# Optimization experiments

Measured on AMD Instinct MI355X. Metric: run time of the kernel, lower is better.

## Reference

```python
import jax, jax.numpy as jnp
import numpy as np

N_NODES = 50000
N_EDGES = 1600000
IN_DIM, HID, HEADS, OUT_DIM = 128, 32, 4, 16
NEG_SLOPE = 0.2  # DGL GATConv default


def setup_inputs() -> dict:
    key = jax.random.key(0)
    ks = jax.random.split(key, 12)
    features = jax.random.normal(ks[0], (N_NODES, IN_DIM), dtype=jnp.float32)
    src = jax.random.randint(ks[1], (N_EDGES,), 0, N_NODES, dtype=jnp.int32)
    dst = jax.random.randint(ks[2], (N_EDGES,), 0, N_NODES, dtype=jnp.int32)
    # layer 1 params (xavier-style scale)
    W1 = jax.random.normal(ks[3], (IN_DIM, HEADS * HID), dtype=jnp.float32) * (2.0 / (IN_DIM + HEADS * HID)) ** 0.5
    al1 = jax.random.normal(ks[4], (HEADS, HID), dtype=jnp.float32) * 0.1
    ar1 = jax.random.normal(ks[5], (HEADS, HID), dtype=jnp.float32) * 0.1
    b1 = jnp.zeros((HEADS * HID,), dtype=jnp.float32)
    # layer 2 params
    W2 = jax.random.normal(ks[6], (HID, OUT_DIM), dtype=jnp.float32) * (2.0 / (HID + OUT_DIM)) ** 0.5
    al2 = jax.random.normal(ks[7], (1, OUT_DIM), dtype=jnp.float32) * 0.1
    ar2 = jax.random.normal(ks[8], (1, OUT_DIM), dtype=jnp.float32) * 0.1
    b2 = jnp.zeros((OUT_DIM,), dtype=jnp.float32)
    return {"features": features, "src": src, "dst": dst,
            "W1": W1, "al1": al1, "ar1": ar1, "b1": b1,
            "W2": W2, "al2": al2, "ar2": ar2, "b2": b2}


def gat_conv(x, src, dst, W, al, ar, b, n_nodes):
    """DGL GATConv (no dropout, no residual). Returns [N, H, out]."""
    H, out = al.shape
    feat = (x @ W).reshape(-1, H, out)                       # [N,H,out]
    el = jnp.sum(feat * al, axis=-1)                         # [N,H]
    er = jnp.sum(feat * ar, axis=-1)                         # [N,H]
    e = jax.nn.leaky_relu(el[src] + er[dst], NEG_SLOPE)      # [E,H]
    # segment softmax over incoming edges per destination node
    m = jax.ops.segment_max(e, dst, num_segments=n_nodes)    # [N,H]
    ex = jnp.exp(e - m[dst])                                 # [E,H]
    s = jax.ops.segment_sum(ex, dst, num_segments=n_nodes)   # [N,H]
    alpha = ex / s[dst]                                      # [E,H]
    msg = alpha[:, :, None] * feat[src]                      # [E,H,out]
    rst = jax.ops.segment_sum(msg, dst, num_segments=n_nodes)
    return rst + b.reshape(H, out)


def reference(features, src, dst, W1, al1, ar1, b1, W2, al2, ar2, b2):
    n = features.shape[0]
    x1 = gat_conv(features, src, dst, W1, al1, ar1, b1, n)   # [N,HEADS,HID]
    x1 = jnp.mean(jax.nn.relu(x1), axis=1)                   # [N,HID]
    x2 = gat_conv(x1, src, dst, W2, al2, ar2, b2, n)         # [N,1,OUT]
    x2 = jnp.squeeze(x2, axis=1)                             # [N,OUT]
    return jax.nn.log_softmax(x2, axis=-1)
```

## Files before the change

kernel.cpp:

```cpp
#include <hip/hip_runtime.h>
#include <math.h>

#define NEG_SLOPE 0.2f
#define BINCAP 10240

typedef __attribute__((ext_vector_type(8))) short short8;
typedef __attribute__((ext_vector_type(4))) float f32x4;

__device__ __forceinline__ float lrelu(float x) {
    return x >= 0.f ? x : NEG_SLOPE * x;
}
__device__ __forceinline__ unsigned bf16_rne(float f) {
    unsigned b = __float_as_uint(f);
    return (b + 0x7FFFu + ((b >> 16) & 1u)) >> 16;
}

__global__ __launch_bounds__(256) void init_cursor(int* __restrict__ bin_cursor) {
    bin_cursor[threadIdx.x] = threadIdx.x * BINCAP;
}

__global__ __launch_bounds__(256) void scatter_bins(
    const int* __restrict__ src, const int* __restrict__ dst,
    int* __restrict__ bin_cursor, unsigned* __restrict__ binned,
    int E, int nbins)
{
    __shared__ int hist[256];
    __shared__ int base_l[256];
    int tid = threadIdx.x;
    hist[tid] = 0;
    __syncthreads();
    int epb = (E + gridDim.x - 1) / gridDim.x;
    int beg = blockIdx.x * epb, end = min(E, beg + epb);
    for (int e = beg + tid; e < end; e += 256)
        atomicAdd(&hist[dst[e] >> 8], 1);
    __syncthreads();
    if (tid < nbins) {
        int c = hist[tid];
        base_l[tid] = (c > 0) ? atomicAdd(&bin_cursor[tid], c) : 0;
    }
    __syncthreads();
    hist[tid] = 0;
    __syncthreads();
    for (int e = beg + tid; e < end; e += 256) {
        int d = dst[e];
        int bin = d >> 8;
        int slot = atomicAdd(&hist[bin], 1);
        binned[base_l[bin] + slot] = ((unsigned)(d & 255) << 16) | (unsigned)src[e];
    }
}

__global__ __launch_bounds__(256) void local_sort(
    const unsigned* __restrict__ binned, const int* __restrict__ bin_cursor,
    int* __restrict__ rowptr, unsigned short* __restrict__ deg,
    unsigned short* __restrict__ csr, int N, int nbins)
{
    __shared__ int cnt[256];
    __shared__ int sh[256];
    int b = blockIdx.x;
    int t = threadIdx.x;
    int gbase = b * BINCAP;
    int gcount = bin_cursor[b] - gbase;
    cnt[t] = 0;
    __syncthreads();
    for (int i = t; i < gcount; i += 256)
        atomicAdd(&cnt[binned[gbase + i] >> 16], 1);
    __syncthreads();
    int own = cnt[t];
    sh[t] = own;
    __syncthreads();
#pragma unroll
    for (int off = 1; off < 256; off <<= 1) {
        int v = (t >= off) ? sh[t - off] : 0;
        __syncthreads();
        sh[t] += v;
        __syncthreads();
    }
    int excl = sh[t] - own;
    int dcount = min(256, N - (b << 8));
    if (t < dcount) {
        rowptr[(b << 8) + t] = gbase + excl;
        deg[(b << 8) + t] = (unsigned short)own;
    }
    cnt[t] = excl;
    __syncthreads();
    for (int i = t; i < gcount; i += 256) {
        unsigned w = binned[gbase + i];
        int slot = atomicAdd(&cnt[w >> 16], 1);
        csr[gbase + slot] = (unsigned short)(w & 0xFFFFu);
    }
}

__global__ __launch_bounds__(256) void convert_w1(
    const float* __restrict__ W, unsigned short* __restrict__ Wt)
{
    int i = blockIdx.x * 256 + threadIdx.x;
    int kin = i >> 7, nout = i & 127;
    Wt[nout * 128 + kin] = (unsigned short)bf16_rne(W[kin * 128 + nout]);
}

__global__ __launch_bounds__(256) void gemm1_mfma(
    const float* __restrict__ X, const unsigned short* __restrict__ Wt,
    unsigned short* __restrict__ feat1b, int N)
{
    __shared__ unsigned short Xb[64][136];
    __shared__ unsigned short Wb[128][136];
    int tid = threadIdx.x;
    int nb = blockIdx.x * 64;

    for (int idx = tid; idx < 128 * 16; idx += 256) {
        int row = idx >> 4, q = idx & 15;
        *(uint4*)&Wb[row][q * 8] = *(const uint4*)&Wt[row * 128 + q * 8];
    }
    for (int idx = tid; idx < 64 * 32; idx += 256) {
        int row = idx >> 5, q = idx & 31;
        int n = nb + row;
        float4 v = (n < N) ? *(const float4*)&X[(size_t)n * 128 + q * 4]
                           : make_float4(0.f, 0.f, 0.f, 0.f);
        unsigned lo = bf16_rne(v.x) | (bf16_rne(v.y) << 16);
        unsigned hi = bf16_rne(v.z) | (bf16_rne(v.w) << 16);
        *(uint2*)&Xb[row][q * 4] = make_uint2(lo, hi);
    }
    __syncthreads();

    int wave = tid >> 6, lane = tid & 63;
    int m = lane & 15, quad = lane >> 4;
    f32x4 acc[8];
#pragma unroll
    for (int t = 0; t < 8; ++t) acc[t] = (f32x4){0.f, 0.f, 0.f, 0.f};

#pragma unroll
    for (int kt = 0; kt < 4; ++kt) {
        int k0 = kt * 32 + quad * 8;
        short8 a = *(const short8*)&Xb[wave * 16 + m][k0];
#pragma unroll
        for (int t = 0; t < 8; ++t) {
            short8 b = *(const short8*)&Wb[t * 16 + m][k0];
            acc[t] = __builtin_amdgcn_mfma_f32_16x16x32_bf16(a, b, acc[t], 0, 0, 0);
        }
    }

#pragma unroll
    for (int r = 0; r < 4; ++r) {
        int n = nb + wave * 16 + quad * 4 + r;
        if (n < N) {
#pragma unroll
            for (int t = 0; t < 8; ++t)
                feat1b[(size_t)n * 128 + t * 16 + m] =
                    (unsigned short)bf16_rne(acc[t][r]);
        }
    }
}

__global__ __launch_bounds__(256) void el_er1(
    const unsigned short* __restrict__ feat1b, const float* __restrict__ al,
    const float* __restrict__ ar, float* __restrict__ el1,
    float* __restrict__ er1, int N)
{
    int t = blockIdx.x * 256 + threadIdx.x;
    if (t >= N * 4) return;
    int n = t >> 2, h = t & 3;
    const unsigned* fp = (const unsigned*)(feat1b + (size_t)n * 128 + h * 32);
    const float* alh = al + h * 32;
    const float* arh = ar + h * 32;
    float pel = 0.f, per = 0.f;
#pragma unroll
    for (int q = 0; q < 16; ++q) {
        unsigned u = fp[q];
        float f0 = __uint_as_float(u << 16);
        float f1 = __uint_as_float(u & 0xFFFF0000u);
        pel += f0 * alh[2 * q] + f1 * alh[2 * q + 1];
        per += f0 * arh[2 * q] + f1 * arh[2 * q + 1];
    }
    el1[t] = pel;
    er1[t] = per;
}

__global__ __launch_bounds__(256) void agg1_fused(
    const int* __restrict__ rowptr, const unsigned short* __restrict__ deg,
    const unsigned short* __restrict__ csr,
    const unsigned short* __restrict__ feat1b, const float* __restrict__ el1,
    const float* __restrict__ er1, float* __restrict__ rst1, int N)
{
    __shared__ uint2 pairs[4][4][66];
    int gid = blockIdx.x * 256 + threadIdx.x;
    int d = gid >> 6;
    if (d >= N) return;
    int wv = (threadIdx.x >> 6) & 3;
    int lane = threadIdx.x & 63;
    int h = lane >> 4;
    float4 er4 = ((const float4*)er1)[d];
    int beg = rowptr[d], end = beg + (int)deg[d];
    const unsigned* feat32 = (const unsigned*)feat1b;

    float M = -INFINITY, S = 0.f, a0 = 0.f, a1 = 0.f;

    for (int base = beg; base < end; base += 64) {
        int cnt = min(64, end - base);
        int sn = 0;
        float4 v = make_float4(-INFINITY, -INFINITY, -INFINITY, -INFINITY);
        if (lane < cnt) {
            sn = (int)csr[base + lane];
            float4 el4 = ((const float4*)el1)[sn];
            v.x = lrelu(el4.x + er4.x);
            v.y = lrelu(el4.y + er4.y);
            v.z = lrelu(el4.z + er4.z);
            v.w = lrelu(el4.w + er4.w);
        }
        float4 cm = v;
#pragma unroll
        for (int off = 1; off < 64; off <<= 1) {
            cm.x = fmaxf(cm.x, __shfl_xor(cm.x, off));
            cm.y = fmaxf(cm.y, __shfl_xor(cm.y, off));
            cm.z = fmaxf(cm.z, __shfl_xor(cm.z, off));
            cm.w = fmaxf(cm.w, __shfl_xor(cm.w, off));
        }
        float4 w;
        w.x = __expf(v.x - cm.x);
        w.y = __expf(v.y - cm.y);
        w.z = __expf(v.z - cm.z);
        w.w = __expf(v.w - cm.w);
        unsigned snb = (unsigned)sn << 6;
        pairs[wv][0][lane] = make_uint2(snb, __float_as_uint(w.x));
        pairs[wv][1][lane] = make_uint2(snb, __float_as_uint(w.y));
        pairs[wv][2][lane] = make_uint2(snb, __float_as_uint(w.z));
        pairs[wv][3][lane] = make_uint2(snb, __float_as_uint(w.w));

        float cmh = (h & 2) ? ((h & 1) ? cm.w : cm.z) : ((h & 1) ? cm.y : cm.x);
        float nM = fmaxf(M, cmh);
        float so = __expf(M - nM);
        float sc = __expf(cmh - nM);
        M = nM;

        float ca0 = 0.f, ca1 = 0.f, cs = 0.f;
        for (int i = 0; i < cnt; ++i) {
            uint2 p = pairs[wv][h][i];
            float wb = __uint_as_float(p.y);
            unsigned u = feat32[p.x + lane];
            float f0 = __uint_as_float(u << 16);
            float f1 = __uint_as_float(u & 0xFFFF0000u);
            ca0 += wb * f0;
            ca1 += wb * f1;
            cs += wb;
        }
        S = S * so + cs * sc;
        a0 = a0 * so + ca0 * sc;
        a1 = a1 * so + ca1 * sc;
    }
    float inv = (end > beg) ? (1.f / S) : 0.f;
    float2* o = (float2*)(rst1 + (size_t)d * 128 + lane * 2);
    *o = make_float2(a0 * inv, a1 * inv);
}

__global__ __launch_bounds__(256) void node_mid(
    const float* __restrict__ rst1, const float* __restrict__ b1,
    const float* __restrict__ W2, const float* __restrict__ al2,
    const float* __restrict__ ar2,
    float* __restrict__ feat2, float* __restrict__ el2, float* __restrict__ er2,
    int N)
{
    int n = blockIdx.x * 256 + threadIdx.x;
    if (n >= N) return;
    float x1[32];
#pragma unroll
    for (int d = 0; d < 32; ++d) x1[d] = 0.f;
    const float4* row = (const float4*)(rst1 + (size_t)n * 128);
#pragma unroll
    for (int hh = 0; hh < 4; ++hh) {
#pragma unroll
        for (int q = 0; q < 8; ++q) {
            float4 v = row[hh * 8 + q];
            float4 bb = *(const float4*)(b1 + hh * 32 + q * 4);
            x1[q * 4 + 0] += fmaxf(v.x + bb.x, 0.f);
            x1[q * 4 + 1] += fmaxf(v.y + bb.y, 0.f);
            x1[q * 4 + 2] += fmaxf(v.z + bb.z, 0.f);
            x1[q * 4 + 3] += fmaxf(v.w + bb.w, 0.f);
        }
    }
#pragma unroll
    for (int d = 0; d < 32; ++d) x1[d] *= 0.25f;

    float f2[16];
#pragma unroll
    for (int j = 0; j < 16; ++j) f2[j] = 0.f;
#pragma unroll
    for (int d = 0; d < 32; ++d) {
        float xv = x1[d];
        const float4* w = (const float4*)(W2 + d * 16);
#pragma unroll
        for (int q = 0; q < 4; ++q) {
            float4 wv = w[q];
            f2[q * 4 + 0] += xv * wv.x;
            f2[q * 4 + 1] += xv * wv.y;
            f2[q * 4 + 2] += xv * wv.z;
            f2[q * 4 + 3] += xv * wv.w;
        }
    }
    float4* o = (float4*)(feat2 + (size_t)n * 16);
#pragma unroll
    for (int q = 0; q < 4; ++q)
        o[q] = make_float4(f2[q * 4 + 0], f2[q * 4 + 1], f2[q * 4 + 2], f2[q * 4 + 3]);
    float el = 0.f, er = 0.f;
#pragma unroll
    for (int j = 0; j < 16; ++j) {
        el += f2[j] * al2[j];
        er += f2[j] * ar2[j];
    }
    el2[n] = el;
    er2[n] = er;
}

__global__ __launch_bounds__(256) void agg2_fused(
    const int* __restrict__ rowptr, const unsigned short* __restrict__ deg,
    const unsigned short* __restrict__ csr,
    const float* __restrict__ feat2, const float* __restrict__ el2,
    const float* __restrict__ er2, const float* __restrict__ b2,
    float* __restrict__ out, int N)
{
    __shared__ uint2 pairs2[4][4][18];
    int gid = blockIdx.x * 256 + threadIdx.x;
    int d = gid >> 4;
    if (d >= N) return;
    int tid = threadIdx.x;
    int wv = (tid >> 6) & 3;
    int grp = (tid >> 4) & 3;
    int l16 = tid & 15;
    float er = er2[d];
    int beg = rowptr[d], end = beg + (int)deg[d];

    float M = -INFINITY, S = 0.f, a = 0.f;
    for (int cb = beg; cb < end; cb += 16) {
        int cnt = min(16, end - cb);
        int sn = 0;
        float v = -INFINITY;
        if (l16 < cnt) {
            sn = (int)csr[cb + l16];
            v = lrelu(el2[sn] + er);
        }
        float cm = v;
#pragma unroll
        for (int off = 1; off < 16; off <<= 1)
            cm = fmaxf(cm, __shfl_xor(cm, off));
        float w = __expf(v - cm);
        pairs2[wv][grp][l16] = make_uint2((unsigned)sn << 4, __float_as_uint(w));
        float nM = fmaxf(M, cm);
        float so = __expf(M - nM);
        float sc = __expf(cm - nM);
        M = nM;
        float ca = 0.f, cs = 0.f;
        for (int i = 0; i < cnt; ++i) {
            uint2 p = pairs2[wv][grp][i];
            float wb = __uint_as_float(p.y);
            float f = feat2[p.x + l16];
            ca += wb * f;
            cs += wb;
        }
        S = S * so + cs * sc;
        a = a * so + ca * sc;
    }
    float inv = (end > beg) ? (1.f / S) : 0.f;
    float val = a * inv + b2[l16];
    float mm = val;
#pragma unroll
    for (int off = 1; off < 16; off <<= 1)
        mm = fmaxf(mm, __shfl_xor(mm, off));
    float ex = __expf(val - mm);
    float ssum = ex;
#pragma unroll
    for (int off = 1; off < 16; off <<= 1)
        ssum += __shfl_xor(ssum, off);
    out[(size_t)d * 16 + l16] = val - (mm + __logf(ssum));
}

extern "C" void kernel_launch(void* const* d_in, const int* in_sizes, int n_in,
                              void* d_out, int out_size, void* d_ws, size_t ws_size,
                              hipStream_t stream)
{
    const float* X   = (const float*)d_in[0];
    const int*   src = (const int*)d_in[1];
    const int*   dst = (const int*)d_in[2];
    const float* W1  = (const float*)d_in[3];
    const float* al1 = (const float*)d_in[4];
    const float* ar1 = (const float*)d_in[5];
    const float* b1  = (const float*)d_in[6];
    const float* W2  = (const float*)d_in[7];
    const float* al2 = (const float*)d_in[8];
    const float* ar2 = (const float*)d_in[9];
    const float* b2  = (const float*)d_in[10];
    int N = in_sizes[0] / 128;
    int E = in_sizes[1];
    int nbins = (N + 255) >> 8;

    float* ws = (float*)d_ws;
    size_t o = 0;
    unsigned short* feat1b = (unsigned short*)(ws + o); o += (size_t)N * 64;
    float* rst1  = ws + o; o += (size_t)N * 128;
    float* el1   = ws + o; o += (size_t)N * 4;
    float* er1   = ws + o; o += (size_t)N * 4;
    float* feat2 = ws + o; o += (size_t)N * 16;
    float* el2   = ws + o; o += (size_t)N;
    float* er2   = ws + o; o += (size_t)N;
    int* rowptr  = (int*)(ws + o); o += (size_t)N;
    unsigned short* deg = (unsigned short*)(ws + o); o += (size_t)N / 2 + 1;
    unsigned short* Wt1b = (unsigned short*)(ws + o); o += 128 * 128 / 2;
    int* bin_cursor = (int*)(ws + o); o += 256;
    unsigned* binned = (unsigned*)(ws + o); o += (size_t)nbins * BINCAP;
    unsigned short* csr = (unsigned short*)(ws + o); o += (size_t)nbins * BINCAP / 2 + 1;
    float* out = (float*)d_out;

    init_cursor<<<1, 256, 0, stream>>>(bin_cursor);
    scatter_bins<<<256, 256, 0, stream>>>(src, dst, bin_cursor, binned, E, nbins);
    local_sort<<<nbins, 256, 0, stream>>>(binned, bin_cursor, rowptr, deg, csr, N, nbins);

    convert_w1<<<64, 256, 0, stream>>>(W1, Wt1b);
    gemm1_mfma<<<(N + 63) / 64, 256, 0, stream>>>(X, Wt1b, feat1b, N);
    el_er1<<<(N * 4 + 255) / 256, 256, 0, stream>>>(feat1b, al1, ar1, el1, er1, N);
    agg1_fused<<<(N * 64 + 255) / 256, 256, 0, stream>>>(rowptr, deg, csr, feat1b, el1, er1, rst1, N);

    node_mid<<<(N + 255) / 256, 256, 0, stream>>>(rst1, b1, W2, al2, ar2, feat2, el2, er2, N);
    agg2_fused<<<(N * 16 + 255) / 256, 256, 0, stream>>>(rowptr, deg, csr, feat2, el2, er2, b2, out, N);
}
```

Before: 252.9 us.

## Fuse node_mid into agg1 epilogue and store layer-2 features as bf16

Folds the bias, ReLU, head-mean, W2 projection and el2/er2 computation into the tail of agg1_fused using wave shuffles. This drops one kernel launch and the 25.6MB round trip of the rst1 buffer. The layer-2 features are now stored as bf16, which halves the gather traffic in agg2. The cost is some extra shuffle and FMA work per destination and lower precision in feat2.

```diff
diff --git a/kernel.cpp b/kernel.cpp
--- a/kernel.cpp
+++ b/kernel.cpp
@@ -179,7 +179,10 @@
     const int* __restrict__ rowptr, const unsigned short* __restrict__ deg,
     const unsigned short* __restrict__ csr,
     const unsigned short* __restrict__ feat1b, const float* __restrict__ el1,
-    const float* __restrict__ er1, float* __restrict__ rst1, int N)
+    const float* __restrict__ er1, const float* __restrict__ b1,
+    const float* __restrict__ W2, const float* __restrict__ al2,
+    const float* __restrict__ ar2, unsigned short* __restrict__ feat2b,
+    float* __restrict__ el2, float* __restrict__ er2, int N)
 {
     __shared__ uint2 pairs[4][4][66];
     int gid = blockIdx.x * 256 + threadIdx.x;
@@ -247,72 +250,39 @@
         a1 = a1 * so + ca1 * sc;
     }
     float inv = (end > beg) ? (1.f / S) : 0.f;
-    float2* o = (float2*)(rst1 + (size_t)d * 128 + lane * 2);
-    *o = make_float2(a0 * inv, a1 * inv);
-}
-
-__global__ __launch_bounds__(256) void node_mid(
-    const float* __restrict__ rst1, const float* __restrict__ b1,
-    const float* __restrict__ W2, const float* __restrict__ al2,
-    const float* __restrict__ ar2,
-    float* __restrict__ feat2, float* __restrict__ el2, float* __restrict__ er2,
-    int N)
-{
-    int n = blockIdx.x * 256 + threadIdx.x;
-    if (n >= N) return;
-    float x1[32];
-#pragma unroll
-    for (int d = 0; d < 32; ++d) x1[d] = 0.f;
-    const float4* row = (const float4*)(rst1 + (size_t)n * 128);
-#pragma unroll
-    for (int hh = 0; hh < 4; ++hh) {
-#pragma unroll
-        for (int q = 0; q < 8; ++q) {
-            float4 v = row[hh * 8 + q];
-            float4 bb = *(const float4*)(b1 + hh * 32 + q * 4);
-            x1[q * 4 + 0] += fmaxf(v.x + bb.x, 0.f);
-            x1[q * 4 + 1] += fmaxf(v.y + bb.y, 0.f);
-            x1[q * 4 + 2] += fmaxf(v.z + bb.z, 0.f);
-            x1[q * 4 + 3] += fmaxf(v.w + bb.w, 0.f);
-        }
-    }
-#pragma unroll
-    for (int d = 0; d < 32; ++d) x1[d] *= 0.25f;
-
-    float f2[16];
-#pragma unroll
-    for (int j = 0; j < 16; ++j) f2[j] = 0.f;
-#pragma unroll
-    for (int d = 0; d < 32; ++d) {
-        float xv = x1[d];
-        const float4* w = (const float4*)(W2 + d * 16);
-#pragma unroll
-        for (int q = 0; q < 4; ++q) {
-            float4 wv = w[q];
-            f2[q * 4 + 0] += xv * wv.x;
-            f2[q * 4 + 1] += xv * wv.y;
-            f2[q * 4 + 2] += xv * wv.z;
-            f2[q * 4 + 3] += xv * wv.w;
-        }
-    }
-    float4* o = (float4*)(feat2 + (size_t)n * 16);
-#pragma unroll
-    for (int q = 0; q < 4; ++q)
-        o[q] = make_float4(f2[q * 4 + 0], f2[q * 4 + 1], f2[q * 4 + 2], f2[q * 4 + 3]);
-    float el = 0.f, er = 0.f;
-#pragma unroll
-    for (int j = 0; j < 16; ++j) {
-        el += f2[j] * al2[j];
-        er += f2[j] * ar2[j];
-    }
-    el2[n] = el;
-    er2[n] = er;
+    float o0 = a0 * inv, o1 = a1 * inv;
+
+    int dim0 = lane * 2;
+    float2 bb = *(const float2*)(b1 + dim0);
+    float r0 = fmaxf(o0 + bb.x, 0.f);
+    float r1 = fmaxf(o1 + bb.y, 0.f);
+    r0 += __shfl_xor(r0, 16); r0 += __shfl_xor(r0, 32);
+    r1 += __shfl_xor(r1, 16); r1 += __shfl_xor(r1, 32);
+    float u0 = 0.25f * r0;
+    float u1 = 0.25f * r1;
+
+    int j = lane & 15;
+    float f2 = 0.f;
+#pragma unroll
+    for (int i = 0; i < 16; ++i) {
+        float xa = __shfl(u0, i);
+        float xb = __shfl(u1, i);
+        f2 += xa * W2[(2 * i) * 16 + j] + xb * W2[(2 * i + 1) * 16 + j];
+    }
+    float pel = f2 * al2[j], per = f2 * ar2[j];
+#pragma unroll
+    for (int off = 1; off < 16; off <<= 1) {
+        pel += __shfl_xor(pel, off);
+        per += __shfl_xor(per, off);
+    }
+    if (lane < 16) feat2b[(size_t)d * 16 + j] = (unsigned short)bf16_rne(f2);
+    if (lane == 0) { el2[d] = pel; er2[d] = per; }
 }
 
 __global__ __launch_bounds__(256) void agg2_fused(
     const int* __restrict__ rowptr, const unsigned short* __restrict__ deg,
     const unsigned short* __restrict__ csr,
-    const float* __restrict__ feat2, const float* __restrict__ el2,
+    const unsigned short* __restrict__ feat2b, const float* __restrict__ el2,
     const float* __restrict__ er2, const float* __restrict__ b2,
     float* __restrict__ out, int N)
 {
@@ -350,7 +320,8 @@
         for (int i = 0; i < cnt; ++i) {
             uint2 p = pairs2[wv][grp][i];
             float wb = __uint_as_float(p.y);
-            float f = feat2[p.x + l16];
+            unsigned u = (unsigned)feat2b[p.x + l16];
+            float f = __uint_as_float(u << 16);
             ca += wb * f;
             cs += wb;
         }
@@ -393,10 +364,9 @@
     float* ws = (float*)d_ws;
     size_t o = 0;
     unsigned short* feat1b = (unsigned short*)(ws + o); o += (size_t)N * 64;
-    float* rst1  = ws + o; o += (size_t)N * 128;
     float* el1   = ws + o; o += (size_t)N * 4;
     float* er1   = ws + o; o += (size_t)N * 4;
-    float* feat2 = ws + o; o += (size_t)N * 16;
+    unsigned short* feat2b = (unsigned short*)(ws + o); o += (size_t)N * 8;
     float* el2   = ws + o; o += (size_t)N;
     float* er2   = ws + o; o += (size_t)N;
     int* rowptr  = (int*)(ws + o); o += (size_t)N;
@@ -414,8 +384,10 @@
     convert_w1<<<64, 256, 0, stream>>>(W1, Wt1b);
     gemm1_mfma<<<(N + 63) / 64, 256, 0, stream>>>(X, Wt1b, feat1b, N);
     el_er1<<<(N * 4 + 255) / 256, 256, 0, stream>>>(feat1b, al1, ar1, el1, er1, N);
-    agg1_fused<<<(N * 64 + 255) / 256, 256, 0, stream>>>(rowptr, deg, csr, feat1b, el1, er1, rst1, N);
-
-    node_mid<<<(N + 255) / 256, 256, 0, stream>>>(rst1, b1, W2, al2, ar2, feat2, el2, er2, N);
-    agg2_fused<<<(N * 16 + 255) / 256, 256, 0, stream>>>(rowptr, deg, csr, feat2, el2, er2, b2, out, N);
-}
+
+    agg1_fused<<<(N * 64 + 255) / 256, 256, 0, stream>>>(
+        rowptr, deg, csr, feat1b, el1, er1, b1, W2, al2, ar2, feat2b, el2, er2, N);
+
+    agg2_fused<<<(N * 16 + 255) / 256, 256, 0, stream>>>(
+        rowptr, deg, csr, feat2b, el2, er2, b2, out, N);
+}
```

Result: no change. 250.9 us (-0.8%).
